# Kernel optimization log

Measured on AMD Instinct MI355X. Metric: run time of the kernel, lower is better.

The kernel has to match this reference:

```python
import jax, jax.numpy as jnp
import numpy as np

HIDDEN_DIM = 2048
N = 4  # expansion_rate
LAYER_IDX = 0
S_ALPHA = 0.01
S_BETA = 0.01
EPS = 1e-5


def setup_inputs() -> dict:
    key = jax.random.key(0)
    k1, k2, k3, k4, k5 = jax.random.split(key, 5)
    batch, seq = 4, 2048
    layer_output = jax.random.normal(k1, (batch, seq, HIDDEN_DIM), dtype=jnp.float32)
    hidden_states = jax.random.normal(k2, (batch, seq, N, HIDDEN_DIM), dtype=jnp.float32)
    # static base matrices (initialization from the torch module)
    B = jnp.ones((1, N), dtype=jnp.float32)
    Am = jnp.zeros((N, 1), dtype=jnp.float32).at[LAYER_IDX % N, 0].set(1.0)
    Ar = jnp.eye(N, dtype=jnp.float32)
    # dynamic parameters
    s_alpha = jnp.full((N, N), S_ALPHA, dtype=jnp.float32)
    s_beta = jnp.full((1, N), S_BETA, dtype=jnp.float32)
    W_beta = jax.random.normal(k3, (HIDDEN_DIM, N), dtype=jnp.float32) * 0.02
    W_m = jax.random.normal(k4, (HIDDEN_DIM, N), dtype=jnp.float32) * 0.02
    W_r = jax.random.normal(k5, (HIDDEN_DIM, N, N), dtype=jnp.float32) * 0.02
    return {
        "layer_output": layer_output,
        "hidden_states": hidden_states,
        "B": B,
        "Am": Am,
        "Ar": Ar,
        "s_alpha": s_alpha,
        "s_beta": s_beta,
        "W_beta": W_beta,
        "W_m": W_m,
        "W_r": W_r,
    }


def reference(layer_output, hidden_states, B, Am, Ar, s_alpha, s_beta, W_beta, W_m, W_r):
    # hidden_states: [b, s, n, d]; layer_output: [b, s, d]
    # --- dynamic matrices ---
    mu = jnp.mean(hidden_states, axis=-1, keepdims=True)
    var = jnp.var(hidden_states, axis=-1, keepdims=True)
    H_norm = (hidden_states - mu) * jax.lax.rsqrt(var + EPS)  # layer_norm, no affine
    H_bar = H_norm.mean(axis=2)  # [b, s, d]

    delta_B = jnp.tanh(H_bar @ W_beta)            # [b, s, n]
    B_dyn = s_beta[0] * delta_B + B[0]            # [b, s, n]
    delta_Am = jnp.tanh(H_bar @ W_m)              # [b, s, n]
    Am_dyn = s_alpha[:, 0] * delta_Am + Am[:, 0]  # [b, s, n]
    delta_Ar = jnp.tanh(jnp.einsum('bsd,dij->bsij', H_bar, W_r))  # [b, s, n, n]
    Ar_dyn = s_alpha * delta_Ar + Ar              # [b, s, n, n]

    # --- combine ---
    depth = B_dyn[..., None] * layer_output[:, :, None, :]                       # [b,s,n,d]
    mixed = jnp.einsum('bsn,bsnd->bsd', Am_dyn, hidden_states)[:, :, None, :]    # [b,s,1,d] broadcasts over n
    residual = jnp.einsum('bsij,bsjd->bsid', Ar_dyn, hidden_states)              # [b,s,n,d]
    return depth + mixed + residual
```

## Files before the change

### kernel.cpp

```cpp
#include <hip/hip_runtime.h>
#include <hip/hip_fp16.h>

#define D     2048
#define BLK   512
#define EPSV  1e-5f

typedef _Float16 h2 __attribute__((ext_vector_type(2)));

__device__ __forceinline__ unsigned int pkh(float a, float b) {
    return __builtin_bit_cast(unsigned int, __builtin_amdgcn_cvt_pkrtz(a, b));
}
__device__ __forceinline__ h2 ash2(unsigned int u) {
    return __builtin_bit_cast(h2, u);
}

template<int CTRL>
__device__ __forceinline__ float dppadd(float x) {
    int y = __builtin_amdgcn_update_dpp(0, __builtin_bit_cast(int, x), CTRL, 0xf, 0xf, false);
    return x + __builtin_bit_cast(float, y);
}
__device__ __forceinline__ float wave_sum(float x) {
    x += __shfl_xor(x, 32, 64);
    x += __shfl_xor(x, 16, 64);
    x = dppadd<0x111>(x);
    x = dppadd<0x112>(x);
    x = dppadd<0x114>(x);
    x = dppadd<0x118>(x);
    return x;
}

__device__ __forceinline__ float rdlane(float v, int l) {
    return __builtin_bit_cast(float, __builtin_amdgcn_readlane(__builtin_bit_cast(int, v), l));
}

__global__ __launch_bounds__(256) void wt_kernel(
    const float* __restrict__ Wb, const float* __restrict__ Wm,
    const float* __restrict__ Wr, unsigned int* __restrict__ Wq,
    float* __restrict__ S)
{
    const int c = blockIdx.x;
    const int t = threadIdx.x;
    const float* src;
    int stride;
    if (c < 4)       { src = Wb + c;       stride = 4;  }
    else if (c < 8)  { src = Wm + (c - 4); stride = 4;  }
    else             { src = Wr + (c - 8); stride = 16; }

    float s = 0.f;
    #pragma unroll
    for (int k = 0; k < 4; ++k) {
        int p = t + 256 * k;
        float a = src[(2 * p)     * stride];
        float b = src[(2 * p + 1) * stride];
        s += a + b;
        Wq[c * 1024 + p] = pkh(a, b);
    }
    __shared__ float rsum[4];
    #pragma unroll
    for (int off = 32; off; off >>= 1) s += __shfl_xor(s, off, 64);
    if ((t & 63) == 0) rsum[t >> 6] = s;
    __syncthreads();
    if (t == 0) S[c] = rsum[0] + rsum[1] + rsum[2] + rsum[3];
}

__global__ __launch_bounds__(BLK) void hc_kernel(
    const float* __restrict__ lo,
    const float* __restrict__ hs,
    const float* __restrict__ Bm,
    const float* __restrict__ Am,
    const float* __restrict__ Ar,
    const float* __restrict__ s_alpha,
    const float* __restrict__ s_beta,
    const unsigned int* __restrict__ Wq,
    const float* __restrict__ S,
    float* __restrict__ out)
{
    __shared__ __align__(16) unsigned int hq[4][1024];
    __shared__ float Rl[24][4];
    __shared__ float sred[8][2];

    const int tid  = threadIdx.x;
    const int wave = tid >> 6;
    const int lane = tid & 63;
    const int row  = wave >> 1;
    const int half = wave & 1;
    const long tok = blockIdx.x;

    const float4* hs4  = (const float4*)(hs + tok * (long)(4 * D));
    const float4* lo4  = (const float4*)(lo + tok * (long)D);
    float4*       out4 = (float4*)(out + tok * (long)(4 * D));

    float4 hv[4];
    const int base = row * 512 + half * 256 + lane;
    #pragma unroll
    for (int k = 0; k < 4; ++k) hv[k] = hs4[base + 64 * k];
    float4 lv = lo4[tid];

    float s = 0.f, q = 0.f;
    uint2* hq2w = (uint2*)hq[row];
    #pragma unroll
    for (int k = 0; k < 4; ++k) {
        float4 v = hv[k];
        s += v.x + v.y + v.z + v.w;
        q += v.x * v.x + v.y * v.y + v.z * v.z + v.w * v.w;
        uint2 p;
        p.x = pkh(v.x, v.y);
        p.y = pkh(v.z, v.w);
        hq2w[half * 256 + 64 * k + lane] = p;
    }
    s = wave_sum(s);
    q = wave_sum(q);
    if (lane == 15) { sred[wave][0] = s; sred[wave][1] = q; }
    __syncthreads();

    float acc[3][4];
    #pragma unroll
    for (int j = 0; j < 3; ++j)
        #pragma unroll
        for (int n = 0; n < 4; ++n) acc[j][n] = 0.f;

    const int c0 = wave * 3;
    const uint2* Wq2 = (const uint2*)Wq;

    #pragma unroll
    for (int k = 0; k < 8; ++k) {
        int i = 64 * k + lane;
        uint2 hr[4];
        #pragma unroll
        for (int n = 0; n < 4; ++n) hr[n] = ((const uint2*)hq[n])[i];
        uint2 wv[3];
        #pragma unroll
        for (int j = 0; j < 3; ++j) wv[j] = Wq2[(c0 + j) * 512 + i];
        #pragma unroll
        for (int j = 0; j < 3; ++j)
            #pragma unroll
            for (int n = 0; n < 4; ++n) {
                acc[j][n] = __builtin_amdgcn_fdot2(ash2(hr[n].x), ash2(wv[j].x), acc[j][n], false);
                acc[j][n] = __builtin_amdgcn_fdot2(ash2(hr[n].y), ash2(wv[j].y), acc[j][n], false);
            }
    }
    #pragma unroll
    for (int j = 0; j < 3; ++j)
        #pragma unroll
        for (int n = 0; n < 4; ++n) {
            float v = wave_sum(acc[j][n]);
            if (lane == 15) Rl[c0 + j][n] = v;
        }
    __syncthreads();

    float cv = 0.f;
    if (lane < 24) {
        int c = lane;
        float Sc = S[c];
        float raw = 0.f;
        #pragma unroll
        for (int n = 0; n < 4; ++n) {
            float ss = sred[2 * n][0] + sred[2 * n + 1][0];
            float qq = sred[2 * n][1] + sred[2 * n + 1][1];
            float m   = ss * (1.f / D);
            float var = qq * (1.f / D) - m * m;
            float r   = rsqrtf(var + EPSV);
            raw += r * (Rl[c][n] - m * Sc);
        }
        raw *= 0.25f;
        float t = tanhf(raw);
        if (c < 4) {
            cv = s_beta[c] * t + Bm[c];
        } else if (c < 8) {
            int n = c - 4;
            cv = s_alpha[n * 4] * t + Am[n];
        } else {
            int ij = c - 8;
            cv = s_alpha[ij] * t + Ar[ij];
        }
    }
    float Bd[4], Amd[4], Ard[4][4];
    #pragma unroll
    for (int n = 0; n < 4; ++n) {
        Bd[n]  = rdlane(cv, n);
        Amd[n] = rdlane(cv, 4 + n);
    }
    #pragma unroll
    for (int i = 0; i < 4; ++i)
        #pragma unroll
        for (int j = 0; j < 4; ++j) Ard[i][j] = rdlane(cv, 8 + i * 4 + j);

    float4 h[4];
    #pragma unroll
    for (int n = 0; n < 4; ++n) {
        uint2 r = ((const uint2*)hq[n])[tid];
        h2 a = ash2(r.x), b = ash2(r.y);
        h[n].x = (float)a[0]; h[n].y = (float)a[1];
        h[n].z = (float)b[0]; h[n].w = (float)b[1];
    }
    float4 mx = {0.f, 0.f, 0.f, 0.f};
    #pragma unroll
    for (int n = 0; n < 4; ++n) {
        mx.x += Amd[n] * h[n].x; mx.y += Amd[n] * h[n].y;
        mx.z += Amd[n] * h[n].z; mx.w += Amd[n] * h[n].w;
    }
    #pragma unroll
    for (int i = 0; i < 4; ++i) {
        float4 o;
        o.x = Bd[i] * lv.x + mx.x;
        o.y = Bd[i] * lv.y + mx.y;
        o.z = Bd[i] * lv.z + mx.z;
        o.w = Bd[i] * lv.w + mx.w;
        #pragma unroll
        for (int j = 0; j < 4; ++j) {
            o.x += Ard[i][j] * h[j].x;
            o.y += Ard[i][j] * h[j].y;
            o.z += Ard[i][j] * h[j].z;
            o.w += Ard[i][j] * h[j].w;
        }
        out4[i * 512 + tid] = o;
    }
}

extern "C" void kernel_launch(void* const* d_in, const int* in_sizes, int n_in,
                              void* d_out, int out_size, void* d_ws, size_t ws_size,
                              hipStream_t stream) {
    const float* lo      = (const float*)d_in[0];
    const float* hs      = (const float*)d_in[1];
    const float* Bm      = (const float*)d_in[2];
    const float* Am      = (const float*)d_in[3];
    const float* Ar      = (const float*)d_in[4];
    const float* s_alpha = (const float*)d_in[5];
    const float* s_beta  = (const float*)d_in[6];
    const float* Wb      = (const float*)d_in[7];
    const float* Wm      = (const float*)d_in[8];
    const float* Wr      = (const float*)d_in[9];
    float* out = (float*)d_out;

    unsigned int* Wq = (unsigned int*)d_ws;
    float* S         = (float*)((char*)d_ws + 24 * 1024 * 4);

    wt_kernel<<<24, 256, 0, stream>>>(Wb, Wm, Wr, Wq, S);

    const int tokens = in_sizes[0] / D;
    hc_kernel<<<tokens, BLK, 0, stream>>>(lo, hs, Bm, Am, Ar, s_alpha, s_beta,
                                          Wq, S, out);
}
```

Before: 143.3 us.

## Fuse projection dot products into hidden-state load loop and use fast tanh

Each wave now computes partial dot products of its own hidden-state slice against all 24 weight columns while loading it from global memory. This removes the separate LDS-read GEMV phase and one block barrier, and partial sums are combined through a small shared table. In exchange it needs 24 accumulators per thread and more global weight loads per wave, and the wave_sum reduction count rises from 12 to 24. tanhf is replaced with an exp/rcp approximation.

```diff
diff --git a/kernel.cpp b/kernel.cpp
--- a/kernel.cpp
+++ b/kernel.cpp
@@ -31,6 +31,12 @@
 
 __device__ __forceinline__ float rdlane(float v, int l) {
     return __builtin_bit_cast(float, __builtin_amdgcn_readlane(__builtin_bit_cast(int, v), l));
+}
+
+__device__ __forceinline__ float ftanh(float x) {
+    float xc = fminf(fmaxf(x, -10.f), 10.f);
+    float e  = __expf(2.f * xc);
+    return 1.f - 2.f * __builtin_amdgcn_rcpf(e + 1.f);
 }
 
 __global__ __launch_bounds__(256) void wt_kernel(
@@ -76,7 +82,7 @@
     float* __restrict__ out)
 {
     __shared__ __align__(16) unsigned int hq[4][1024];
-    __shared__ float Rl[24][4];
+    __shared__ float pred[8][24];
     __shared__ float sred[8][2];
 
     const int tid  = threadIdx.x;
@@ -90,62 +96,43 @@
     const float4* lo4  = (const float4*)(lo + tok * (long)D);
     float4*       out4 = (float4*)(out + tok * (long)(4 * D));
 
-    float4 hv[4];
-    const int base = row * 512 + half * 256 + lane;
-    #pragma unroll
-    for (int k = 0; k < 4; ++k) hv[k] = hs4[base + 64 * k];
-    float4 lv = lo4[tid];
-
+    float acc[24];
+    #pragma unroll
+    for (int c = 0; c < 24; ++c) acc[c] = 0.f;
     float s = 0.f, q = 0.f;
+
     uint2* hq2w = (uint2*)hq[row];
+    const uint2* Wq2 = (const uint2*)Wq;
+    const int kb = half * 256 + lane;
+
     #pragma unroll
     for (int k = 0; k < 4; ++k) {
-        float4 v = hv[k];
+        int i4 = kb + 64 * k;
+        float4 v = hs4[row * 512 + i4];
         s += v.x + v.y + v.z + v.w;
         q += v.x * v.x + v.y * v.y + v.z * v.z + v.w * v.w;
-        uint2 p;
-        p.x = pkh(v.x, v.y);
-        p.y = pkh(v.z, v.w);
-        hq2w[half * 256 + 64 * k + lane] = p;
-    }
+        unsigned int plo_u = pkh(v.x, v.y);
+        unsigned int phi_u = pkh(v.z, v.w);
+        hq2w[i4] = make_uint2(plo_u, phi_u);
+        h2 plo = ash2(plo_u), phi = ash2(phi_u);
+        #pragma unroll
+        for (int c = 0; c < 24; ++c) {
+            uint2 w = Wq2[c * 512 + i4];
+            acc[c] = __builtin_amdgcn_fdot2(plo, ash2(w.x), acc[c], false);
+            acc[c] = __builtin_amdgcn_fdot2(phi, ash2(w.y), acc[c], false);
+        }
+    }
+    float4 lv = lo4[tid];
+
     s = wave_sum(s);
     q = wave_sum(q);
     if (lane == 15) { sred[wave][0] = s; sred[wave][1] = q; }
-    __syncthreads();
-
-    float acc[3][4];
-    #pragma unroll
-    for (int j = 0; j < 3; ++j)
-        #pragma unroll
-        for (int n = 0; n < 4; ++n) acc[j][n] = 0.f;
-
-    const int c0 = wave * 3;
-    const uint2* Wq2 = (const uint2*)Wq;
-
-    #pragma unroll
-    for (int k = 0; k < 8; ++k) {
-        int i = 64 * k + lane;
-        uint2 hr[4];
-        #pragma unroll
-        for (int n = 0; n < 4; ++n) hr[n] = ((const uint2*)hq[n])[i];
-        uint2 wv[3];
-        #pragma unroll
-        for (int j = 0; j < 3; ++j) wv[j] = Wq2[(c0 + j) * 512 + i];
-        #pragma unroll
-        for (int j = 0; j < 3; ++j)
-            #pragma unroll
-            for (int n = 0; n < 4; ++n) {
-                acc[j][n] = __builtin_amdgcn_fdot2(ash2(hr[n].x), ash2(wv[j].x), acc[j][n], false);
-                acc[j][n] = __builtin_amdgcn_fdot2(ash2(hr[n].y), ash2(wv[j].y), acc[j][n], false);
-            }
-    }
-    #pragma unroll
-    for (int j = 0; j < 3; ++j)
-        #pragma unroll
-        for (int n = 0; n < 4; ++n) {
-            float v = wave_sum(acc[j][n]);
-            if (lane == 15) Rl[c0 + j][n] = v;
-        }
+    #pragma unroll
+    for (int c = 0; c < 24; ++c) {
+        float v = wave_sum(acc[c]);
+        if ((lane & 15) == 15 && (c & 3) == (lane >> 4))
+            pred[wave][c] = v;
+    }
     __syncthreads();
 
     float cv = 0.f;
@@ -155,24 +142,19 @@
         float raw = 0.f;
         #pragma unroll
         for (int n = 0; n < 4; ++n) {
+            float R  = pred[2 * n][c] + pred[2 * n + 1][c];
             float ss = sred[2 * n][0] + sred[2 * n + 1][0];
             float qq = sred[2 * n][1] + sred[2 * n + 1][1];
             float m   = ss * (1.f / D);
             float var = qq * (1.f / D) - m * m;
             float r   = rsqrtf(var + EPSV);
-            raw += r * (Rl[c][n] - m * Sc);
+            raw += r * (R - m * Sc);
         }
         raw *= 0.25f;
-        float t = tanhf(raw);
-        if (c < 4) {
-            cv = s_beta[c] * t + Bm[c];
-        } else if (c < 8) {
-            int n = c - 4;
-            cv = s_alpha[n * 4] * t + Am[n];
-        } else {
-            int ij = c - 8;
-            cv = s_alpha[ij] * t + Ar[ij];
-        }
+        float t = ftanh(raw);
+        if (c < 4)      cv = s_beta[c] * t + Bm[c];
+        else if (c < 8) cv = s_alpha[(c - 4) * 4] * t + Am[c - 4];
+        else            cv = s_alpha[c - 8] * t + Ar[c - 8];
     }
     float Bd[4], Amd[4], Ard[4][4];
     #pragma unroll
```

Result: slower. 370.7 us (+158.6%).
